# Optimization experiments

Hardware: AMD Instinct MI355X
Metric: run time of the kernel (lower is better)

The kernel has to match this reference:

```python
import jax, jax.numpy as jnp
import numpy as np

BEV_H, BEV_W, RES, ZH = 50, 50, 0.5, 0.0
IMG_H, IMG_W, STRIDE = 448, 800, 16
FH, FW = IMG_H // STRIDE, IMG_W // STRIDE  # 28, 50
NCAM, D, NL, NHEADS, NPTS = 6, 256, 2, 8, 4
NQ = BEV_H * BEV_W
EPS = 1e-5


def make_bev_grid_points():
    x = (jnp.arange(BEV_H) - (BEV_H - 1) / 2) * RES
    y = (jnp.arange(BEV_W) - (BEV_W - 1) / 2) * RES
    xx, yy = jnp.meshgrid(x, y, indexing='ij')
    return jnp.stack([xx, yy, jnp.full_like(xx, ZH)], -1).reshape(-1, 3)


def layer_norm(x, g, b):
    m = x.mean(-1, keepdims=True)
    v = x.var(-1, keepdims=True)
    return (x - m) / jnp.sqrt(v + EPS) * g + b


def group_norm(x, g, b, groups=32):
    B, C, H, W = x.shape
    xg = x.reshape(B, groups, C // groups, H, W)
    m = xg.mean((2, 3, 4), keepdims=True)
    v = xg.var((2, 3, 4), keepdims=True)
    xg = (xg - m) / jnp.sqrt(v + EPS)
    return xg.reshape(B, C, H, W) * g[None, :, None, None] + b[None, :, None, None]


def conv2d(x, w, b, stride, pad):
    y = jax.lax.conv_general_dilated(x, w, (stride, stride), ((pad, pad), (pad, pad)),
                                     dimension_numbers=('NCHW', 'OIHW', 'NCHW'))
    return y + b[None, :, None, None]


def mha(x, wq, bq, wk, bk, wv, bv, wo, bo):
    B, N, d = x.shape
    hd = d // NHEADS
    split = lambda t: t.reshape(B, N, NHEADS, hd).transpose(0, 2, 1, 3)
    q, k, v = split(x @ wq + bq), split(x @ wk + bk), split(x @ wv + bv)
    a = jax.nn.softmax(jnp.einsum('bhqd,bhkd->bhqk', q, k) * (1.0 / float(np.sqrt(hd))), axis=-1)
    o = jnp.einsum('bhqk,bhkd->bhqd', a, v).transpose(0, 2, 1, 3).reshape(B, N, d)
    return o @ wo + bo


def grid_sample(val, grid):
    # val: [C, Hf, Wf]; grid: [P, 2] in [-1, 1]; bilinear, align_corners=True, zeros padding.
    C, Hf, Wf = val.shape
    gx = (grid[:, 0] + 1.0) * 0.5 * (Wf - 1)
    gy = (grid[:, 1] + 1.0) * 0.5 * (Hf - 1)
    x0 = jnp.floor(gx)
    y0 = jnp.floor(gy)
    wx, wy = gx - x0, gy - y0
    x0i, y0i = x0.astype(jnp.int32), y0.astype(jnp.int32)
    out = jnp.zeros((C, grid.shape[0]), val.dtype)
    for dx, dy, w in ((0, 0, (1 - wx) * (1 - wy)), (1, 0, wx * (1 - wy)),
                      (0, 1, (1 - wx) * wy), (1, 1, wx * wy)):
        xi, yi = x0i + dx, y0i + dy
        ok = ((xi >= 0) & (xi < Wf) & (yi >= 0) & (yi < Hf)).astype(val.dtype)
        feat = val[:, jnp.clip(yi, 0, Hf - 1), jnp.clip(xi, 0, Wf - 1)]  # [C, P]
        out = out + (w * ok)[None, :] * feat
    return out.T  # [P, C]


def project(pts, K, E):
    # pts: [Np,3] ego-frame; K: [B,NCAM,3,3]; E: [B,NCAM,4,4]
    ph = jnp.concatenate([pts, jnp.ones((pts.shape[0], 1), pts.dtype)], -1)
    pc = jnp.einsum('bcij,pj->bcpi', E, ph)              # [B,NCAM,Np,4]
    pix = jnp.einsum('bcij,bcpj->bcpi', K, pc[..., :3])
    z = jnp.clip(pix[..., 2:3], 1e-5, None)
    uv = pix[..., :2] / z
    u, v = uv[..., 0], uv[..., 1]
    valid = (pc[..., 2] > 0) & (u >= 0) & (u < IMG_W) & (v >= 0) & (v < IMG_H)
    uvn = jnp.stack([2.0 * u / (IMG_W - 1) - 1.0, 2.0 * v / (IMG_H - 1) - 1.0], -1)
    return uvn, valid


def spatial_cross_attn(q, feats, ref, valid, ow, ob, ww, wb, vw, vb, pw, pb):
    B, Nq, d = q.shape
    vals = jnp.einsum('bnchw,cd->bndhw', feats, vw) + vb[None, None, :, None, None]
    offsets = (q @ ow + ob).reshape(B, Nq, NCAM, NHEADS, NPTS, 2)
    logits = q @ ww + wb                                  # [B,Nq,NCAM*NHEADS*NPTS]
    mask = jnp.broadcast_to(valid.transpose(0, 2, 1)[..., None],
                            (B, Nq, NCAM, NHEADS * NPTS)).reshape(B, Nq, -1)
    w = jax.nn.softmax(jnp.where(mask, logits, jnp.asarray(-1e30, logits.dtype)), axis=-1)
    w = jnp.where(mask, w, 0.0)  # == masked_fill(-inf) + softmax + nan_to_num(0)
    w = w.reshape(B, Nq, NCAM, NHEADS, NPTS)
    scale = jnp.array([2.0 / (FW - 1), 2.0 / (FH - 1)], q.dtype)
    gs = jax.vmap(grid_sample)
    out = jnp.zeros((B, Nq, d), q.dtype)
    for c in range(NCAM):  # fixed small camera loop, as in original
        pts = ref[:, c][:, :, None, None, :] + offsets[:, :, c] * scale  # [B,Nq,H,K,2]
        sampled = gs(vals[:, c], pts.reshape(B, Nq * NHEADS * NPTS, 2))
        sampled = sampled.reshape(B, Nq, NHEADS, NPTS, d)
        out = out + jnp.einsum('bqhk,bqhkd->bqd', w[:, :, c], sampled)
    return out @ pw + pb


def reference(images, intrinsics, ego_to_cam, bev_queries, bev_pos,
              bb_w0, bb_b0, bb_g0, bb_beta0, bb_w1, bb_b1, bb_g1, bb_beta1,
              bb_w2, bb_b2, bb_g2, bb_beta2, bb_w3, bb_b3, bb_g3, bb_beta3,
              bb_w4, bb_b4, bb_g4, bb_beta4,
              sa_wq, sa_bq, sa_wk, sa_bk, sa_wv, sa_bv, sa_wo, sa_bo,
              ln1_g, ln1_b, ln2_g, ln2_b, ln3_g, ln3_b,
              off_w, off_b, wt_w, wt_b, val_w, val_b, out_w, out_b,
              ffn_w1, ffn_b1, ffn_w2, ffn_b2):
    B = images.shape[0]
    x = images.reshape(B * NCAM, 3, IMG_H, IMG_W)
    for w, b, g, bt in ((bb_w0, bb_b0, bb_g0, bb_beta0), (bb_w1, bb_b1, bb_g1, bb_beta1),
                        (bb_w2, bb_b2, bb_g2, bb_beta2), (bb_w3, bb_b3, bb_g3, bb_beta3)):
        x = jax.nn.relu(group_norm(conv2d(x, w, b, 2, 1), g, bt))
    x = group_norm(conv2d(x, bb_w4, bb_b4, 1, 0), bb_g4, bb_beta4)
    feats = x.reshape(B, NCAM, D, FH, FW)
    ref_pts, valid = project(make_bev_grid_points().astype(images.dtype), intrinsics, ego_to_cam)
    q = jnp.broadcast_to((bev_queries + bev_pos)[None], (B, NQ, D))
    for l in range(NL):
        xq = layer_norm(q, ln1_g[l], ln1_b[l])
        q = q + mha(xq, sa_wq[l], sa_bq[l], sa_wk[l], sa_bk[l], sa_wv[l], sa_bv[l], sa_wo[l], sa_bo[l])
        xq = layer_norm(q, ln2_g[l], ln2_b[l])
        q = q + spatial_cross_attn(xq, feats, ref_pts, valid, off_w[l], off_b[l],
                                   wt_w[l], wt_b[l], val_w[l], val_b[l], out_w[l], out_b[l])
        xq = layer_norm(q, ln3_g[l], ln3_b[l])
        q = q + (jax.nn.gelu(xq @ ffn_w1[l] + ffn_b1[l], approximate=False) @ ffn_w2[l] + ffn_b2[l])
    return q.reshape(B, BEV_H, BEV_W, D)


def _camera_geometry():
    fx = fy = 500.0
    cx, cy = IMG_W / 2.0, IMG_H / 2.0
    K = np.array([[fx, 0, cx], [0, fy, cy], [0, 0, 1]], np.float32)
    Ks, Es = [], []
    for th in np.linspace(0, 2 * np.pi, NCAM, endpoint=False):
        f = np.array([np.cos(th), np.sin(th), 0.0])
        r = np.array([np.sin(th), -np.cos(th), 0.0])
        dn = np.array([0.0, 0.0, -1.0])
        R = np.stack([r, dn, f]).astype(np.float32)
        c = np.array([1.5 * np.cos(th), 1.5 * np.sin(th), 1.5], np.float32)
        E = np.eye(4, dtype=np.float32)
        E[:3, :3] = R
        E[:3, 3] = -R @ c
        Ks.append(K)
        Es.append(E)
    return np.stack(Ks)[None], np.stack(Es)[None]


def setup_inputs() -> dict:
    key = jax.random.key(0)
    ks = iter(jax.random.split(key, 80))
    rn = lambda shape, s: jax.random.normal(next(ks), shape, jnp.float32) * s
    K_np, E_np = _camera_geometry()
    d = {}
    d['images'] = rn((1, NCAM, 3, IMG_H, IMG_W), 1.0)
    d['intrinsics'] = jnp.asarray(K_np)
    d['ego_to_cam'] = jnp.asarray(E_np)
    d['bev_queries'] = rn((NQ, D), 0.02)
    d['bev_pos'] = rn((NQ, D), 0.02)
    for i, (co, ci) in enumerate(((64, 3), (128, 64), (256, 128), (256, 256))):
        d[f'bb_w{i}'] = rn((co, ci, 3, 3), (2.0 / (ci * 9)) ** 0.5)
        d[f'bb_b{i}'] = jnp.zeros((co,))
        d[f'bb_g{i}'] = jnp.ones((co,))
        d[f'bb_beta{i}'] = jnp.zeros((co,))
    d['bb_w4'] = rn((D, D, 1, 1), (2.0 / D) ** 0.5)
    d['bb_b4'] = jnp.zeros((D,)); d['bb_g4'] = jnp.ones((D,)); d['bb_beta4'] = jnp.zeros((D,))
    s = (1.0 / D) ** 0.5
    for n in ('q', 'k', 'v', 'o'):
        d[f'sa_w{n}'] = rn((NL, D, D), s)
        d[f'sa_b{n}'] = jnp.zeros((NL, D))
    for i in (1, 2, 3):
        d[f'ln{i}_g'] = jnp.ones((NL, D))
        d[f'ln{i}_b'] = jnp.zeros((NL, D))
    npw = NCAM * NHEADS * NPTS
    d['off_w'] = rn((NL, D, npw * 2), 0.005)  # original inits zeros; small values exercise sampling
    d['off_b'] = rn((NL, npw * 2), 0.1)
    d['wt_w'] = rn((NL, D, npw), s)
    d['wt_b'] = jnp.zeros((NL, npw))
    d['val_w'] = rn((NL, D, D), s)
    d['val_b'] = jnp.zeros((NL, D))
    d['out_w'] = rn((NL, D, D), s)
    d['out_b'] = jnp.zeros((NL, D))
    d['ffn_w1'] = rn((NL, D, 4 * D), s)
    d['ffn_b1'] = jnp.zeros((NL, 4 * D))
    d['ffn_w2'] = rn((NL, 4 * D, D), (1.0 / (4 * D)) ** 0.5)
    d['ffn_b2'] = jnp.zeros((NL, D))
    return d
```

## Files before the change

kernel.cpp:

```cpp
#include <hip/hip_runtime.h>
#include <hip/hip_bf16.h>
#include <math.h>

#define EPS 1e-5f
#define FL_SPLITS 5
#define FL_KEYS 500

typedef __attribute__((ext_vector_type(8))) short short8;
typedef __attribute__((ext_vector_type(4))) float f4;

__device__ __forceinline__ short f2s(float f) {
    union { float f; unsigned u; } v; v.f = f;
    unsigned r = (v.u + 0x7fffu + ((v.u >> 16) & 1u)) >> 16;
    return (short)r;
}
__device__ __forceinline__ unsigned packbf(float a, float b) {
    return (unsigned)(unsigned short)f2s(a) | ((unsigned)(unsigned short)f2s(b) << 16);
}
__device__ __forceinline__ float bflo(unsigned v) { union { unsigned u; float f; } t; t.u = v << 16; return t.f; }
__device__ __forceinline__ float bfhi(unsigned v) { union { unsigned u; float f; } t; t.u = v & 0xffff0000u; return t.f; }

__global__ __launch_bounds__(256) void wcast_k(const float* __restrict__ in, short* __restrict__ out, int n)
{
    int i = blockIdx.x * 256 + threadIdx.x;
    if (i < n) out[i] = f2s(in[i]);
}

__global__ __launch_bounds__(256) void wcast0_k(const float* __restrict__ in, short* __restrict__ out)
{
    int i = blockIdx.x * 256 + threadIdx.x;
    if (i >= 2048) return;
    int k = i & 31;
    out[i] = (k < 27) ? f2s(in[(i >> 5) * 27 + k]) : (short)0;
}

__global__ __launch_bounds__(256) void wreord_k(const float* __restrict__ in, short* __restrict__ out,
                                                int Cin, int n)
{
    int i = blockIdx.x * 256 + threadIdx.x;
    if (i >= n) return;
    int cin9 = Cin * 9;
    int co = i / cin9, rem = i - co * cin9;
    int ci = rem / 9, t = rem - ci * 9;
    out[(long)co * cin9 + t * Cin + ci] = f2s(in[i]);
}

__global__ __launch_bounds__(256) void wtrans_k(const float* __restrict__ in, short* __restrict__ out,
                                                int K, int N, long zstride)
{
    in  += (long)blockIdx.z * K * N;
    out += (long)blockIdx.z * zstride;
    __shared__ float t[64][65];
    int k0 = blockIdx.y * 64, n0 = blockIdx.x * 64;
    int tid = threadIdx.x;
    int cl = tid & 63, rq = tid >> 6;
    #pragma unroll
    for (int i = 0; i < 16; i++) {
        int rl = rq + i * 4;
        int k = k0 + rl, n = n0 + cl;
        t[rl][cl] = (k < K && n < N) ? in[(long)k * N + n] : 0.f;
    }
    __syncthreads();
    #pragma unroll
    for (int i = 0; i < 16; i++) {
        int nl = rq + i * 4;
        int n = n0 + nl, k = k0 + cl;
        if (n < N && k < K) out[(long)n * K + k] = f2s(t[cl][nl]);
    }
}

__global__ __launch_bounds__(256) void wtrans6_k(const float* __restrict__ s0, const float* __restrict__ s1,
                                                 const float* __restrict__ s2, const float* __restrict__ s3,
                                                 const float* __restrict__ s4, const float* __restrict__ s5,
                                                 short* __restrict__ d0, short* __restrict__ d1,
                                                 short* __restrict__ d2, short* __restrict__ d3,
                                                 short* __restrict__ d4, short* __restrict__ d5)
{
    int mat = blockIdx.z >> 1, l = blockIdx.z & 1;
    const float* in; short* out; long zs;
    if      (mat == 0) { in = s0; out = d0; zs = 196608; }
    else if (mat == 1) { in = s1; out = d1; zs = 196608; }
    else if (mat == 2) { in = s2; out = d2; zs = 196608; }
    else if (mat == 3) { in = s3; out = d3; zs = 65536; }
    else if (mat == 4) { in = s4; out = d4; zs = 65536; }
    else               { in = s5; out = d5; zs = 65536; }
    in  += (long)l * 65536;
    out += (long)l * zs;
    __shared__ float t[64][65];
    int k0 = blockIdx.y * 64, n0 = blockIdx.x * 64;
    int tid = threadIdx.x;
    int cl = tid & 63, rq = tid >> 6;
    #pragma unroll
    for (int i = 0; i < 16; i++) {
        int rl = rq + i * 4;
        t[rl][cl] = in[(long)(k0 + rl) * 256 + n0 + cl];
    }
    __syncthreads();
    #pragma unroll
    for (int i = 0; i < 16; i++) {
        int nl = rq + i * 4;
        out[(long)(n0 + nl) * 256 + k0 + cl] = f2s(t[cl][nl]);
    }
}

__global__ __launch_bounds__(256) void packb_k(const float* __restrict__ a, const float* __restrict__ b,
                                               const float* __restrict__ c, float* __restrict__ y,
                                               int na, int nb, int nc)
{
    int l = blockIdx.y;
    int j = blockIdx.x * 256 + threadIdx.x;
    int ntot = na + nb + nc;
    if (j >= ntot) return;
    float v;
    if (j < na) v = a[l * na + j];
    else if (j < na + nb) v = b[l * nb + (j - na)];
    else v = c[l * nc + (j - na - nb)];
    y[(long)l * ntot + j] = v;
}

__global__ __launch_bounds__(256) void mgemm_k(const float* __restrict__ A, int lda,
                                               const short* __restrict__ Bt,
                                               const float* __restrict__ bias,
                                               const float* __restrict__ resid,
                                               float* __restrict__ C,
                                               int M, int N, int K, int act)
{
    __shared__ __align__(16) short As[2560];
    __shared__ __align__(16) short Bs[2560];
    int tid = threadIdx.x;
    int wave = tid >> 6, lane = tid & 63;
    int wm = wave >> 1, wn = wave & 1;
    int quad = lane >> 4, l15 = lane & 15;
    int m0 = blockIdx.y * 64, n0 = blockIdx.x * 64;
    int srow = tid >> 2, skc = (tid & 3) << 3;
    f4 acc[2][2];
    #pragma unroll
    for (int i = 0; i < 2; i++) { acc[i][0] = (f4){0.f,0.f,0.f,0.f}; acc[i][1] = (f4){0.f,0.f,0.f,0.f}; }
    short8 aR, bR;
    auto loadAB = [&](int kt) {
        int gm = m0 + srow;
        short8 pk = {0, 0, 0, 0, 0, 0, 0, 0};
        if (gm < M) {
            const float4* ap = (const float4*)(A + (long)gm * lda + kt + skc);
            float4 v0 = ap[0], v1 = ap[1];
            pk[0] = f2s(v0.x); pk[1] = f2s(v0.y); pk[2] = f2s(v0.z); pk[3] = f2s(v0.w);
            pk[4] = f2s(v1.x); pk[5] = f2s(v1.y); pk[6] = f2s(v1.z); pk[7] = f2s(v1.w);
        }
        aR = pk;
        int gn = n0 + srow;
        short8 pb = {0, 0, 0, 0, 0, 0, 0, 0};
        if (gn < N) pb = *(const short8*)&Bt[(long)gn * K + kt + skc];
        bR = pb;
    };
    loadAB(0);
    for (int kt = 0; kt < K; kt += 32) {
        *(short8*)&As[srow * 40 + skc] = aR;
        *(short8*)&Bs[srow * 40 + skc] = bR;
        __syncthreads();
        if (kt + 32 < K) loadAB(kt + 32);
        short8 af[2], bf[2];
        #pragma unroll
        for (int mi = 0; mi < 2; mi++) af[mi] = *(const short8*)&As[(wm * 32 + mi * 16 + l15) * 40 + (quad << 3)];
        #pragma unroll
        for (int ni = 0; ni < 2; ni++) bf[ni] = *(const short8*)&Bs[(wn * 32 + ni * 16 + l15) * 40 + (quad << 3)];
        #pragma unroll
        for (int mi = 0; mi < 2; mi++)
            #pragma unroll
            for (int ni = 0; ni < 2; ni++)
                acc[mi][ni] = __builtin_amdgcn_mfma_f32_16x16x32_bf16(af[mi], bf[ni], acc[mi][ni], 0, 0, 0);
        __syncthreads();
    }
    #pragma unroll
    for (int mi = 0; mi < 2; mi++) {
        int row = m0 + wm * 32 + mi * 16 + quad * 4;
        #pragma unroll
        for (int ni = 0; ni < 2; ni++) {
            int col = n0 + wn * 32 + ni * 16 + l15;
            if (col >= N) continue;
            float bv = bias[col];
            #pragma unroll
            for (int r = 0; r < 4; r++) {
                int rr = row + r;
                if (rr >= M) continue;
                float v = acc[mi][ni][r] + bv;
                if (act == 2) v = 0.5f * v * (1.f + erff(v * 0.70710678118654752f));
                if (resid) v += resid[(long)rr * N + col];
                C[(long)rr * N + col] = v;
            }
        }
    }
}

__global__ __launch_bounds__(256) void mconv_k(const unsigned* __restrict__ in,
                                               const short* __restrict__ wgt,
                                               const float* __restrict__ bias,
                                               float* __restrict__ out,
                                               float2* __restrict__ parts,
                                               int c5m, int Cout, int Hin, int Win,
                                               int mode, int cpg,
                                               long istride, long ostride)
{
    in  += (long)blockIdx.z * istride;
    const int Hout = Hin >> 1, Wout = Win >> 1;
    const int HWo = Hout * Wout;
    const int HW = Hin * Win;
    const int Ktot = 288 << c5m;
    const int m5 = (1 << c5m) - 1;
    const int nsteps = 9 << c5m;
    __shared__ __align__(16) short As[2560];
    __shared__ __align__(16) short Bs[2560];
    __shared__ float2 sred[16][2];
    int tid = threadIdx.x;
    int wave = tid >> 6, lane = tid & 63;
    int wm = wave >> 1, wn = wave & 1;
    int quad = lane >> 4, l15 = lane & 15;
    int m0 = blockIdx.y * 64, n0 = blockIdx.x * 64;
    int nn = tid & 63;
    int kp0 = tid >> 6;
    int p = n0 + nn;
    int pok = p < HWo;
    int pc = pok ? p : (HWo - 1);
    int ho = pc / Wout, wo = pc - ho * Wout;
    int hb = ho * 2 - 1, wb = wo * 2 - 1;

    f4 acc[2][2];
    #pragma unroll
    for (int i = 0; i < 2; i++) { acc[i][0] = (f4){0.f,0.f,0.f,0.f}; acc[i][1] = (f4){0.f,0.f,0.f,0.f}; }

    short8 aR;
    unsigned bR[4];
    auto loadA = [&](int s) {
        int r = tid >> 2, kc = (tid & 3) << 3;
        aR = *(const short8*)&wgt[(long)(m0 + r) * Ktot + (s << 5) + kc];
    };
    auto loadB = [&](int s) {
        int t = s >> c5m;
        int kh = (t * 11) >> 5;
        int kw = t - kh * 3;
        int y = hb + kh, x = wb + kw;
        bool okp = pok && ((unsigned)y < (unsigned)Hin) && ((unsigned)x < (unsigned)Win);
        int base = (((s & m5) << 4) + kp0) * HW + y * Win + x;
        #pragma unroll
        for (int i = 0; i < 4; i++) {
            unsigned v = 0;
            if (okp) v = in[base + (i << 2) * HW];
            bR[i] = v;
        }
    };

    loadA(0); loadB(0);
    for (int s = 0; s < nsteps; s++) {
        {
            int r = tid >> 2, kc = (tid & 3) << 3;
            *(short8*)&As[r * 40 + kc] = aR;
        }
        #pragma unroll
        for (int i = 0; i < 4; i++)
            *(unsigned*)&Bs[nn * 40 + ((kp0 + (i << 2)) << 1)] = bR[i];
        __syncthreads();
        if (s + 1 < nsteps) { loadA(s + 1); loadB(s + 1); }
        short8 af[2], bf[2];
        #pragma unroll
        for (int mi = 0; mi < 2; mi++) af[mi] = *(const short8*)&As[(wm * 32 + mi * 16 + l15) * 40 + (quad << 3)];
        #pragma unroll
        for (int ni = 0; ni < 2; ni++) bf[ni] = *(const short8*)&Bs[(wn * 32 + ni * 16 + l15) * 40 + (quad << 3)];
        #pragma unroll
        for (int mi = 0; mi < 2; mi++)
            #pragma unroll
            for (int ni = 0; ni < 2; ni++)
                acc[mi][ni] = __builtin_amdgcn_mfma_f32_16x16x32_bf16(af[mi], bf[ni], acc[mi][ni], 0, 0, 0);
        __syncthreads();
    }

    if (mode == 1) {
        float* outf = out + (long)blockIdx.z * ostride;
        #pragma unroll
        for (int mi = 0; mi < 2; mi++) {
            int mbase = m0 + wm * 32 + mi * 16 + quad * 4;
            #pragma unroll
            for (int ni = 0; ni < 2; ni++) {
                int n = n0 + wn * 32 + ni * 16 + l15;
                if (n >= HWo) continue;
                #pragma unroll
                for (int r = 0; r < 4; r++) {
                    int m = mbase + r;
                    outf[(long)n * Cout + m] = acc[mi][ni][r] + bias[m];
                }
            }
        }
    } else {
        unsigned* outp = (unsigned*)out + (long)blockIdx.z * ostride;
        float ssum[2] = {0.f, 0.f}, qsum[2] = {0.f, 0.f};
        #pragma unroll
        for (int mi = 0; mi < 2; mi++) {
            int mbase = m0 + wm * 32 + mi * 16 + quad * 4;
            float b0 = bias[mbase], b1 = bias[mbase + 1], b2 = bias[mbase + 2], b3 = bias[mbase + 3];
            #pragma unroll
            for (int ni = 0; ni < 2; ni++) {
                int n = n0 + wn * 32 + ni * 16 + l15;
                if (n >= HWo) continue;
                float v0 = acc[mi][ni][0] + b0;
                float v1 = acc[mi][ni][1] + b1;
                float v2 = acc[mi][ni][2] + b2;
                float v3 = acc[mi][ni][3] + b3;
                long cp = (long)(mbase >> 1) * HWo + n;
                outp[cp]       = packbf(v0, v1);
                outp[cp + HWo] = packbf(v2, v3);
                ssum[mi] += v0 + v1 + v2 + v3;
                qsum[mi] += v0 * v0 + v1 * v1 + v2 * v2 + v3 * v3;
            }
        }
        #pragma unroll
        for (int mi = 0; mi < 2; mi++) {
            #pragma unroll
            for (int off = 1; off < 16; off <<= 1) {
                ssum[mi] += __shfl_xor(ssum[mi], off, 16);
                qsum[mi] += __shfl_xor(qsum[mi], off, 16);
            }
        }
        if (l15 == 0) {
            #pragma unroll
            for (int mi = 0; mi < 2; mi++)
                sred[wm * 8 + mi * 4 + quad][wn] = make_float2(ssum[mi], qsum[mi]);
        }
        __syncthreads();
        int ng = 64 / cpg;
        int qpg = cpg >> 2;
        if (tid < ng) {
            float s = 0.f, q = 0.f;
            for (int u = 0; u < qpg; u++) {
                float2 a = sred[(tid * cpg >> 2) + u][0];
                float2 b = sred[(tid * cpg >> 2) + u][1];
                s += a.x + b.x; q += a.y + b.y;
            }
            int gabs = m0 / cpg + tid;
            parts[((long)blockIdx.z * 32 + gabs) * 1400 + blockIdx.x] = make_float2(s, q);
        }
    }
}

__global__ __launch_bounds__(256) void conv0f_k(const float* __restrict__ img,
                                                const short* __restrict__ wgt,
                                                const float* __restrict__ bias,
                                                unsigned* __restrict__ outp,
                                                float2* __restrict__ parts,
                                                long istride, long ostride)
{
    img  += (long)blockIdx.z * istride;
    outp += (long)blockIdx.z * ostride;
    const int HWo = 89600;
    __shared__ __align__(16) short As[2560];
    __shared__ __align__(16) short Bs[2560];
    __shared__ float2 sred[32][2];
    int tid = threadIdx.x;
    int wave = tid >> 6, lane = tid & 63;
    int wm = wave >> 1, wn = wave & 1;
    int quad = lane >> 4, l15 = lane & 15;
    int n0 = blockIdx.x * 64;
    int srow = tid >> 2, skc = (tid & 3) << 3;
    *(short8*)&As[srow * 40 + skc] = *(const short8*)&wgt[srow * 32 + skc];
    {
        int p = n0 + srow;
        int ho = p / 400, wo = p - ho * 400;
        int hb = ho * 2 - 1, wb = wo * 2 - 1;
        short8 pb;
        #pragma unroll
        for (int j = 0; j < 8; j++) {
            int k = skc + j;
            float v = 0.f;
            if (k < 27) {
                int ci = (k < 9) ? 0 : (k < 18 ? 1 : 2);
                int t = k - ci * 9;
                int kh = (t < 3) ? 0 : (t < 6 ? 1 : 2);
                int kw = t - kh * 3;
                int y = hb + kh, x = wb + kw;
                if ((unsigned)y < 448u && (unsigned)x < 800u)
                    v = img[ci * 358400 + y * 800 + x];
            }
            pb[j] = f2s(v);
        }
        *(short8*)&Bs[srow * 40 + skc] = pb;
    }
    __syncthreads();
    f4 acc[2][2];
    #pragma unroll
    for (int i = 0; i < 2; i++) { acc[i][0] = (f4){0.f,0.f,0.f,0.f}; acc[i][1] = (f4){0.f,0.f,0.f,0.f}; }
    short8 af[2], bf[2];
    #pragma unroll
    for (int mi = 0; mi < 2; mi++) af[mi] = *(const short8*)&As[(wm * 32 + mi * 16 + l15) * 40 + (quad << 3)];
    #pragma unroll
    for (int ni = 0; ni < 2; ni++) bf[ni] = *(const short8*)&Bs[(wn * 32 + ni * 16 + l15) * 40 + (quad << 3)];
    #pragma unroll
    for (int mi = 0; mi < 2; mi++)
        #pragma unroll
        for (int ni = 0; ni < 2; ni++)
            acc[mi][ni] = __builtin_amdgcn_mfma_f32_16x16x32_bf16(af[mi], bf[ni], acc[mi][ni], 0, 0, 0);
    #pragma unroll
    for (int mi = 0; mi < 2; mi++) {
        int mbase = wm * 32 + mi * 16 + quad * 4;
        float b0 = bias[mbase], b1 = bias[mbase + 1], b2 = bias[mbase + 2], b3 = bias[mbase + 3];
        float s0 = 0.f, q0 = 0.f, s1 = 0.f, q1 = 0.f;
        #pragma unroll
        for (int ni = 0; ni < 2; ni++) {
            int n = n0 + wn * 32 + ni * 16 + l15;
            float v0 = acc[mi][ni][0] + b0;
            float v1 = acc[mi][ni][1] + b1;
            float v2 = acc[mi][ni][2] + b2;
            float v3 = acc[mi][ni][3] + b3;
            long cp = (long)(mbase >> 1) * HWo + n;
            outp[cp]       = packbf(v0, v1);
            outp[cp + HWo] = packbf(v2, v3);
            s0 += v0 + v1; q0 += v0 * v0 + v1 * v1;
            s1 += v2 + v3; q1 += v2 * v2 + v3 * v3;
        }
        #pragma unroll
        for (int off = 1; off < 16; off <<= 1) {
            s0 += __shfl_xor(s0, off, 16); q0 += __shfl_xor(q0, off, 16);
            s1 += __shfl_xor(s1, off, 16); q1 += __shfl_xor(q1, off, 16);
        }
        if (l15 == 0) {
            int pi = wm * 16 + mi * 8 + quad * 2;
            sred[pi][wn]     = make_float2(s0, q0);
            sred[pi + 1][wn] = make_float2(s1, q1);
        }
    }
    __syncthreads();
    if (tid < 32) {
        float2 a = sred[tid][0], b = sred[tid][1];
        parts[((long)blockIdx.z * 32 + tid) * 1400 + blockIdx.x] = make_float2(a.x + b.x, a.y + b.y);
    }
}

__global__ __launch_bounds__(256) void gnfin_k(const float2* __restrict__ parts,
                                               float* __restrict__ gnstats, int nx, float invN)
{
    int g = blockIdx.x, cam = blockIdx.y;
    const float2* pb = parts + ((long)cam * 32 + g) * 1400;
    float s = 0.f, q = 0.f;
    for (int i = threadIdx.x; i < nx; i += 256) {
        float2 v = pb[i];
        s += v.x; q += v.y;
    }
    __shared__ float rs[256], rq[256];
    rs[threadIdx.x] = s; rq[threadIdx.x] = q;
    __syncthreads();
    for (int o = 128; o > 0; o >>= 1) {
        if (threadIdx.x < o) { rs[threadIdx.x] += rs[threadIdx.x + o]; rq[threadIdx.x] += rq[threadIdx.x + o]; }
        __syncthreads();
    }
    if (threadIdx.x == 0) {
        float mean = rs[0] * invN;
        float var  = rq[0] * invN - mean * mean;
        gnstats[(cam * 32 + g) * 2]     = mean;
        gnstats[(cam * 32 + g) * 2 + 1] = rsqrtf(var + EPS);
    }
}

__global__ __launch_bounds__(256) void pairapply_k(unsigned* __restrict__ x,
                                                   const float* __restrict__ gamma,
                                                   const float* __restrict__ beta,
                                                   const float* __restrict__ gnstats,
                                                   int HW, int cpg, long zstride)
{
    x       += (long)blockIdx.z * zstride;
    gnstats += (long)blockIdx.z * 64;
    int idx4 = (blockIdx.x * 256 + threadIdx.x) * 4;
    int cp = idx4 / HW;
    int c0 = cp * 2;
    int g = c0 / cpg;
    float mean = gnstats[g * 2], rstd = gnstats[g * 2 + 1];
    float sa = rstd * gamma[c0],     ba = beta[c0]     - mean * sa;
    float sb = rstd * gamma[c0 + 1], bb = beta[c0 + 1] - mean * sb;
    uint4 v = *(uint4*)&x[idx4];
    unsigned* vp = (unsigned*)&v;
    #pragma unroll
    for (int j = 0; j < 4; j++) {
        float lo = fmaxf(bflo(vp[j]) * sa + ba, 0.f);
        float hi = fmaxf(bfhi(vp[j]) * sb + bb, 0.f);
        vp[j] = packbf(lo, hi);
    }
    *(uint4*)&x[idx4] = v;
}

__global__ __launch_bounds__(256) void gn_stats_hwd_k(const float* __restrict__ x, float* __restrict__ stats)
{
    x += (long)blockIdx.y * 358400;
    stats += blockIdx.y * 64;
    int g = blockIdx.x;
    float s = 0.f, s2 = 0.f;
    for (int i = threadIdx.x; i < 1400 * 8; i += blockDim.x) {
        int p = i >> 3, c = g * 8 + (i & 7);
        float v = x[(long)p * 256 + c];
        s += v; s2 += v * v;
    }
    __shared__ float rs[256], rq[256];
    rs[threadIdx.x] = s; rq[threadIdx.x] = s2;
    __syncthreads();
    for (int o = 128; o > 0; o >>= 1) {
        if (threadIdx.x < o) { rs[threadIdx.x] += rs[threadIdx.x + o]; rq[threadIdx.x] += rq[threadIdx.x + o]; }
        __syncthreads();
    }
    if (threadIdx.x == 0) {
        float mean = rs[0] / 11200.f;
        float var  = rq[0] / 11200.f - mean * mean;
        stats[g * 2]     = mean;
        stats[g * 2 + 1] = rsqrtf(var + EPS);
    }
}

__global__ __launch_bounds__(256) void gn_apply_hwd_k(float* __restrict__ x,
                                                      const float* __restrict__ gamma,
                                                      const float* __restrict__ beta,
                                                      const float* __restrict__ stats,
                                                      int relu)
{
    x += (long)blockIdx.y * 358400;
    stats += blockIdx.y * 64;
    long i4 = ((long)blockIdx.x * 256 + threadIdx.x) * 4;
    int c = (int)(i4 & 255);
    int g = c >> 3;
    float4 v  = *(float4*)&x[i4];
    float4 gm = *(const float4*)&gamma[c];
    float4 bt = *(const float4*)&beta[c];
    float m = stats[g * 2], rs = stats[g * 2 + 1];
    v.x = (v.x - m) * rs * gm.x + bt.x;
    v.y = (v.y - m) * rs * gm.y + bt.y;
    v.z = (v.z - m) * rs * gm.z + bt.z;
    v.w = (v.w - m) * rs * gm.w + bt.w;
    if (relu) {
        v.x = fmaxf(v.x, 0.f); v.y = fmaxf(v.y, 0.f);
        v.z = fmaxf(v.z, 0.f); v.w = fmaxf(v.w, 0.f);
    }
    *(float4*)&x[i4] = v;
}

__global__ __launch_bounds__(256) void project_k(const float* __restrict__ Kin,
                                                 const float* __restrict__ Ein,
                                                 float* __restrict__ refp, int* __restrict__ valid)
{
    int idx = blockIdx.x * blockDim.x + threadIdx.x;
    if (idx >= 2500 * 6) return;
    int c = idx % 6, q = idx / 6;
    int i = q / 50, j = q % 50;
    float px = (i - 24.5f) * 0.5f;
    float py = (j - 24.5f) * 0.5f;
    const float* E = Ein + c * 16;
    float pc[4];
    #pragma unroll
    for (int r = 0; r < 4; r++)
        pc[r] = E[r * 4 + 0] * px + E[r * 4 + 1] * py + E[r * 4 + 3];
    const float* Km = Kin + c * 9;
    float pix[3];
    #pragma unroll
    for (int r = 0; r < 3; r++)
        pix[r] = Km[r * 3 + 0] * pc[0] + Km[r * 3 + 1] * pc[1] + Km[r * 3 + 2] * pc[2];
    float z = fmaxf(pix[2], 1e-5f);
    float u = pix[0] / z, v = pix[1] / z;
    int ok = (pc[2] > 0.f) && (u >= 0.f) && (u < 800.f) && (v >= 0.f) && (v < 448.f);
    refp[(long)idx * 2 + 0] = 2.f * u / 799.f - 1.f;
    refp[(long)idx * 2 + 1] = 2.f * v / 447.f - 1.f;
    valid[idx] = ok;
}

__global__ __launch_bounds__(256) void qinit_k(const float* __restrict__ a, const float* __restrict__ b,
                                               float* __restrict__ y)
{
    int i = blockIdx.x * blockDim.x + threadIdx.x;
    if (i >= 2500 * 256) return;
    y[i] = a[i] + b[i];
}

__global__ __launch_bounds__(256) void ln_k(const float* __restrict__ x,
                                            const float* __restrict__ g, const float* __restrict__ b,
                                            float* __restrict__ y)
{
    int row  = blockIdx.x * 4 + (threadIdx.x >> 6);
    int lane = threadIdx.x & 63;
    if (row >= 2500) return;
    const float* xp = x + (long)row * 256;
    float v[4];
    #pragma unroll
    for (int i = 0; i < 4; i++) v[i] = xp[lane + 64 * i];
    float s  = v[0] + v[1] + v[2] + v[3];
    float s2 = v[0] * v[0] + v[1] * v[1] + v[2] * v[2] + v[3] * v[3];
    #pragma unroll
    for (int o = 32; o > 0; o >>= 1) { s += __shfl_xor(s, o, 64); s2 += __shfl_xor(s2, o, 64); }
    float mean = s * (1.f / 256.f);
    float var  = s2 * (1.f / 256.f) - mean * mean;
    float rstd = rsqrtf(var + EPS);
    #pragma unroll
    for (int i = 0; i < 4; i++) {
        int cc = lane + 64 * i;
        y[(long)row * 256 + cc] = (v[i] - mean) * rstd * g[cc] + b[cc];
    }
}

__global__ __launch_bounds__(256) void flash2_k(const float* __restrict__ Q,
                                                const float* __restrict__ K,
                                                const float* __restrict__ V,
                                                int ld,
                                                float* __restrict__ Opart,
                                                float* __restrict__ MLpart)
{
    const int h  = blockIdx.y;
    const int q0 = blockIdx.x * 64;
    const int sp = blockIdx.z;
    const int kstart = sp * FL_KEYS, kend = kstart + FL_KEYS;
    const int tid = threadIdx.x;
    const int wave = tid >> 6, lane = tid & 63;
    const int quad = lane >> 4, l15 = lane & 15;
    __shared__ __align__(16) short Qs[64 * 40];
    __shared__ __align__(16) short Ks[64 * 40];
    __shared__ __align__(16) short Vt[32 * 72];
    __shared__ __align__(16) short Ps[64 * 72];
    const float scale = 0.17677669529663687f;
    {
        int row = tid >> 2, kc = (tid & 3) << 3;
        int qi = q0 + row;
        short8 pk = {0, 0, 0, 0, 0, 0, 0, 0};
        if (qi < 2500) {
            const float4* qp = (const float4*)(Q + (long)qi * ld + h * 32 + kc);
            float4 v0 = qp[0], v1 = qp[1];
            pk[0] = f2s(v0.x * scale); pk[1] = f2s(v0.y * scale); pk[2] = f2s(v0.z * scale); pk[3] = f2s(v0.w * scale);
            pk[4] = f2s(v1.x * scale); pk[5] = f2s(v1.y * scale); pk[6] = f2s(v1.z * scale); pk[7] = f2s(v1.w * scale);
        }
        *(short8*)&Qs[row * 40 + kc] = pk;
    }
    __syncthreads();
    short8 aq = *(const short8*)&Qs[(wave * 16 + l15) * 40 + (quad << 3)];
    float m[4], l[4];
    f4 oacc[2];
    #pragma unroll
    for (int r = 0; r < 4; r++) { m[r] = -INFINITY; l[r] = 0.f; }
    oacc[0] = (f4){0.f, 0.f, 0.f, 0.f};
    oacc[1] = (f4){0.f, 0.f, 0.f, 0.f};
    for (int kb = kstart; kb < kend; kb += 64) {
        __syncthreads();
        {
            int row = tid >> 2, kc = (tid & 3) << 3;
            int ki = kb + row;
            short8 pk = {0, 0, 0, 0, 0, 0, 0, 0};
            float vv[8] = {0.f, 0.f, 0.f, 0.f, 0.f, 0.f, 0.f, 0.f};
            if (ki < kend) {
                const float4* kp = (const float4*)(K + (long)ki * ld + h * 32 + kc);
                float4 a0 = kp[0], a1 = kp[1];
                pk[0] = f2s(a0.x); pk[1] = f2s(a0.y); pk[2] = f2s(a0.z); pk[3] = f2s(a0.w);
                pk[4] = f2s(a1.x); pk[5] = f2s(a1.y); pk[6] = f2s(a1.z); pk[7] = f2s(a1.w);
                const float4* vp = (const float4*)(V + (long)ki * ld + h * 32 + kc);
                float4 b0 = vp[0], b1 = vp[1];
                vv[0] = b0.x; vv[1] = b0.y; vv[2] = b0.z; vv[3] = b0.w;
                vv[4] = b1.x; vv[5] = b1.y; vv[6] = b1.z; vv[7] = b1.w;
            }
            *(short8*)&Ks[row * 40 + kc] = pk;
            #pragma unroll
            for (int j = 0; j < 8; j++) Vt[(kc + j) * 72 + row] = f2s(vv[j]);
        }
        __syncthreads();
        f4 sa[4];
        #pragma unroll
        for (int ni = 0; ni < 4; ni++) {
            short8 bk = *(const short8*)&Ks[(ni * 16 + l15) * 40 + (quad << 3)];
            sa[ni] = __builtin_amdgcn_mfma_f32_16x16x32_bf16(aq, bk, (f4){0.f, 0.f, 0.f, 0.f}, 0, 0, 0);
        }
        float sv[4][4];
        #pragma unroll
        for (int ni = 0; ni < 4; ni++) {
            bool colok = (kb + ni * 16 + l15) < kend;
            #pragma unroll
            for (int r = 0; r < 4; r++) sv[ni][r] = colok ? sa[ni][r] : -1e30f;
        }
        float p[4][4];
        #pragma unroll
        for (int r = 0; r < 4; r++) {
            float rm = fmaxf(fmaxf(sv[0][r], sv[1][r]), fmaxf(sv[2][r], sv[3][r]));
            #pragma unroll
            for (int off = 1; off < 16; off <<= 1) rm = fmaxf(rm, __shfl_xor(rm, off, 16));
            float mn = fmaxf(m[r], rm);
            float alpha = __expf(m[r] - mn);
            float rs = 0.f;
            #pragma unroll
            for (int ni = 0; ni < 4; ni++) { p[ni][r] = __expf(sv[ni][r] - mn); rs += p[ni][r]; }
            #pragma unroll
            for (int off = 1; off < 16; off <<= 1) rs += __shfl_xor(rs, off, 16);
            l[r] = l[r] * alpha + rs;
            oacc[0][r] *= alpha; oacc[1][r] *= alpha;
            m[r] = mn;
        }
        #pragma unroll
        for (int ni = 0; ni < 4; ni++)
            #pragma unroll
            for (int r = 0; r < 4; r++)
                Ps[(wave * 16 + quad * 4 + r) * 72 + ni * 16 + l15] = f2s(p[ni][r]);
        #pragma unroll
        for (int kh = 0; kh < 2; kh++) {
            short8 ap = *(const short8*)&Ps[(wave * 16 + l15) * 72 + kh * 32 + (quad << 3)];
            #pragma unroll
            for (int ni = 0; ni < 2; ni++) {
                short8 bv = *(const short8*)&Vt[(ni * 16 + l15) * 72 + kh * 32 + (quad << 3)];
                oacc[ni] = __builtin_amdgcn_mfma_f32_16x16x32_bf16(ap, bv, oacc[ni], 0, 0, 0);
            }
        }
    }
    #pragma unroll
    for (int r = 0; r < 4; r++) {
        int qi = q0 + wave * 16 + quad * 4 + r;
        if (qi < 2500) {
            long ob = ((long)sp * 2500 + qi) * 256 + h * 32;
            Opart[ob + l15]      = oacc[0][r];
            Opart[ob + 16 + l15] = oacc[1][r];
            if (l15 == 0) {
                long mb = (((long)sp * 2500 + qi) * 8 + h) * 2;
                MLpart[mb]     = m[r];
                MLpart[mb + 1] = l[r];
            }
        }
    }
}

__global__ __launch_bounds__(256) void flashmerge_k(const float* __restrict__ Opart,
                                                    const float* __restrict__ MLpart,
                                                    float* __restrict__ O)
{
    int q = blockIdx.x, d = threadIdx.x;
    int h = d >> 5;
    float ms[FL_SPLITS], ls[FL_SPLITS];
    float mg = -INFINITY;
    #pragma unroll
    for (int s = 0; s < FL_SPLITS; s++) {
        long mb = (((long)s * 2500 + q) * 8 + h) * 2;
        ms[s] = MLpart[mb];
        ls[s] = MLpart[mb + 1];
        mg = fmaxf(mg, ms[s]);
    }
    float lsum = 0.f, osum = 0.f;
    #pragma unroll
    for (int s = 0; s < FL_SPLITS; s++) {
        float w = __expf(ms[s] - mg);
        lsum += ls[s] * w;
        osum += Opart[((long)s * 2500 + q) * 256 + d] * w;
    }
    O[(long)q * 256 + d] = osum / lsum;
}

__global__ __launch_bounds__(64) void scasoftmax_k(float* __restrict__ logits, int ld,
                                                   const int* __restrict__ valid)
{
    int q = blockIdx.x, lane = threadIdx.x;
    float v[3]; int mk[3];
    #pragma unroll
    for (int i = 0; i < 3; i++) {
        int idx = i * 64 + lane;
        int c = idx >> 5;
        mk[i] = valid[q * 6 + c];
        v[i] = mk[i] ? logits[(long)q * ld + idx] : -1e30f;
    }
    float mx = fmaxf(fmaxf(v[0], v[1]), v[2]);
    #pragma unroll
    for (int o = 32; o > 0; o >>= 1) mx = fmaxf(mx, __shfl_xor(mx, o, 64));
    float e[3]; float s = 0.f;
    #pragma unroll
    for (int i = 0; i < 3; i++) { e[i] = expf(v[i] - mx); s += e[i]; }
    #pragma unroll
    for (int o = 32; o > 0; o >>= 1) s += __shfl_xor(s, o, 64);
    float inv = 1.f / s;
    #pragma unroll
    for (int i = 0; i < 3; i++)
        logits[(long)q * ld + i * 64 + lane] = mk[i] ? e[i] * inv : 0.f;
}

__global__ __launch_bounds__(256) void sample_k(const float* __restrict__ vals,
                                                const float* __restrict__ offs, int ld,
                                                const float* __restrict__ wts,
                                                const float* __restrict__ refp,
                                                const int* __restrict__ valid,
                                                float* __restrict__ out)
{
    int q = blockIdx.x, d = threadIdx.x;
    __shared__ float s_cw[6][32][4];
    __shared__ int   s_idx[6][32][4];
    if (d < 192) {
        int c = d >> 5, pt = d & 31;
        if (valid[q * 6 + c]) {
            float ox = offs[(long)q * ld + (c * 32 + pt) * 2 + 0];
            float oy = offs[(long)q * ld + (c * 32 + pt) * 2 + 1];
            float px = refp[(q * 6 + c) * 2 + 0] + ox * (2.f / 49.f);
            float py = refp[(q * 6 + c) * 2 + 1] + oy * (2.f / 27.f);
            float gx = (px + 1.f) * 0.5f * 49.f;
            float gy = (py + 1.f) * 0.5f * 27.f;
            float x0f = floorf(gx), y0f = floorf(gy);
            float wx = gx - x0f, wy = gy - y0f;
            int x0 = (int)x0f, y0 = (int)y0f;
            float wgt = wts[(long)q * ld + c * 32 + pt];
            float cw[4] = {(1.f - wx) * (1.f - wy), wx * (1.f - wy), (1.f - wx) * wy, wx * wy};
            const int dxs[4] = {0, 1, 0, 1};
            const int dys[4] = {0, 0, 1, 1};
            #pragma unroll
            for (int k2 = 0; k2 < 4; k2++) {
                int xi = x0 + dxs[k2], yi = y0 + dys[k2];
                bool ok = (xi >= 0) && (xi < 50) && (yi >= 0) && (yi < 28);
                s_cw[c][pt][k2]  = ok ? cw[k2] * wgt : 0.f;
                s_idx[c][pt][k2] = ok ? (yi * 50 + xi) * 256 : 0;
            }
        }
    }
    __syncthreads();
    float acc = 0.f;
    for (int c = 0; c < 6; c++) {
        if (!valid[q * 6 + c]) continue;
        const float* vb = vals + (long)c * 358400 + d;
        for (int pt = 0; pt < 32; pt++) {
            #pragma unroll
            for (int k2 = 0; k2 < 4; k2++) {
                float cwv = s_cw[c][pt][k2];
                if (cwv != 0.f) acc += cwv * vb[s_idx[c][pt][k2]];
            }
        }
    }
    out[(long)q * 256 + d] = acc;
}

extern "C" void kernel_launch(void* const* d_in, const int* in_sizes, int n_in,
                              void* d_out, int out_size, void* d_ws, size_t ws_size,
                              hipStream_t stream)
{
    const float* images = (const float*)d_in[0];
    const float* intr   = (const float*)d_in[1];
    const float* e2c    = (const float*)d_in[2];
    const float* bevq   = (const float*)d_in[3];
    const float* bevp   = (const float*)d_in[4];
    const float* bbw[5]    = {(const float*)d_in[5],  (const float*)d_in[9],  (const float*)d_in[13], (const float*)d_in[17], (const float*)d_in[21]};
    const float* bbb[5]    = {(const float*)d_in[6],  (const float*)d_in[10], (const float*)d_in[14], (const float*)d_in[18], (const float*)d_in[22]};
    const float* bbg[5]    = {(const float*)d_in[7],  (const float*)d_in[11], (const float*)d_in[15], (const float*)d_in[19], (const float*)d_in[23]};
    const float* bbbeta[5] = {(const float*)d_in[8],  (const float*)d_in[12], (const float*)d_in[16], (const float*)d_in[20], (const float*)d_in[24]};
    const float* sa_wq = (const float*)d_in[25]; const float* sa_bq = (const float*)d_in[26];
    const float* sa_wk = (const float*)d_in[27]; const float* sa_bk = (const float*)d_in[28];
    const float* sa_wv = (const float*)d_in[29]; const float* sa_bv = (const float*)d_in[30];
    const float* sa_wo = (const float*)d_in[31]; const float* sa_bo = (const float*)d_in[32];
    const float* ln1g = (const float*)d_in[33]; const float* ln1b = (const float*)d_in[34];
    const float* ln2g = (const float*)d_in[35]; const float* ln2b = (const float*)d_in[36];
    const float* ln3g = (const float*)d_in[37]; const float* ln3b = (const float*)d_in[38];
    const float* offw = (const float*)d_in[39]; const float* offb = (const float*)d_in[40];
    const float* wtw  = (const float*)d_in[41]; const float* wtb  = (const float*)d_in[42];
    const float* valw = (const float*)d_in[43]; const float* valb = (const float*)d_in[44];
    const float* outw = (const float*)d_in[45]; const float* outb = (const float*)d_in[46];
    const float* fw1  = (const float*)d_in[47]; const float* fb1  = (const float*)d_in[48];
    const float* fw2  = (const float*)d_in[49]; const float* fb2  = (const float*)d_in[50];

    auto needB = [](long ncb) -> unsigned long long {
        return (unsigned long long)(ncb * 8601600L + 6681600L) * 4ULL + 6307840ULL + (1 << 20);
    };
    int ncb = 1;
    if      ((unsigned long long)ws_size >= needB(6)) ncb = 6;
    else if ((unsigned long long)ws_size >= needB(3)) ncb = 3;
    else if ((unsigned long long)ws_size >= needB(2)) ncb = 2;

    float* ws = (float*)d_ws;
    float* A     = ws; ws += (long)ncb * 5734400;
    float* Bu    = ws; ws += (long)ncb * 2867200;
    float* f3bH  = ws; ws += 2560000;
    float* feats = ws; ws += 2150400;
    float* qbuf  = ws; ws += 640000;
    float* xq    = ws; ws += 640000;
    float* bO    = ws; ws += 640000;
    float* refp  = ws; ws += 30016;
    int*   validb = (int*)ws; ws += 15040;
    float* stats = ws; ws += 384;
    float* gnst  = ws; ws += 3072;
    float* qkvb  = ws; ws += 1536;
    float* owb   = ws; ws += 1152;
    short* sb = (short*)ws;
    short* cw0b = sb; sb += 2048;
    short* cw1b = sb; sb += 73728;
    short* cw2b = sb; sb += 294912;
    short* cw3b = sb; sb += 589824;
    short* cw4b = sb; sb += 65536;
    short* qkvT = sb; sb += 393216;
    short* owT  = sb; sb += 131072;
    short* valT = sb; sb += 131072;
    short* outT = sb; sb += 131072;
    short* offwtT = sb; sb += 294912;
    short* f1T  = sb; sb += 524288;
    short* f2T  = sb; sb += 524288;
    float*  feats3 = f3bH;
    float*  bH     = f3bH;
    float*  bQKV   = A;
    float*  OP     = A + 1920000;
    float*  bOW    = A + 1920000;
    float*  valsb  = Bu;
    float*  MLp    = Bu + 2150400;
    unsigned* Bbf0 = (unsigned*)A;
    unsigned* Bbf1 = (unsigned*)Bu;
    float2* partsP = (float2*)feats;

    auto mgemm = [&](const float* Ain, int lda, const short* Bt, const float* bias, const float* resid,
                     float* C, int M, int N, int K, int act) {
        dim3 g((N + 63) / 64, (M + 63) / 64);
        mgemm_k<<<g, 256, 0, stream>>>(Ain, lda, Bt, bias, resid, C, M, N, K, act);
    };

    wcast0_k<<<8, 256, 0, stream>>>(bbw[0], cw0b);
    wreord_k<<<(73728 + 255) / 256, 256, 0, stream>>>(bbw[1], cw1b, 64, 73728);
    wreord_k<<<(294912 + 255) / 256, 256, 0, stream>>>(bbw[2], cw2b, 128, 294912);
    wreord_k<<<(589824 + 255) / 256, 256, 0, stream>>>(bbw[3], cw3b, 256, 589824);
    wcast_k<<<(65536 + 255) / 256, 256, 0, stream>>>(bbw[4], cw4b, 65536);
    wtrans6_k<<<dim3(4, 4, 12), 256, 0, stream>>>(sa_wq, sa_wk, sa_wv, sa_wo, valw, outw,
                                                  qkvT, qkvT + 65536, qkvT + 131072, owT, valT, outT);
    wtrans_k<<<dim3(6, 4, 2), 256, 0, stream>>>(offw, offwtT,         256, 384,  147456);
    wtrans_k<<<dim3(3, 4, 2), 256, 0, stream>>>(wtw,  offwtT + 98304, 256, 192,  147456);
    wtrans_k<<<dim3(16, 4, 2), 256, 0, stream>>>(fw1, f1T, 256, 1024, 262144);
    wtrans_k<<<dim3(4, 16, 2), 256, 0, stream>>>(fw2, f2T, 1024, 256, 262144);
    packb_k<<<dim3(3, 2), 256, 0, stream>>>(sa_bq, sa_bk, sa_bv, qkvb, 256, 256, 256);
    packb_k<<<dim3(3, 2), 256, 0, stream>>>(offb, wtb, nullptr, owb, 384, 192, 0);

    project_k<<<(15000 + 255) / 256, 256, 0, stream>>>(intr, e2c, refp, validb);

    for (int c0 = 0; c0 < 6; c0 += ncb) {
        const float* img = images + (long)c0 * 1075200;
        conv0f_k<<<dim3(1400, 1, ncb), 256, 0, stream>>>(img, cw0b, bbb[0], Bbf0, partsP,
                                                         1075200L, 2867200L);
        gnfin_k<<<dim3(32, ncb), 256, 0, stream>>>(partsP, gnst, 1400, 1.f / 179200.f);
        pairapply_k<<<dim3(2800, 1, ncb), 256, 0, stream>>>(Bbf0, bbg[0], bbbeta[0], gnst, 89600, 2, 2867200L);
        mconv_k<<<dim3(350, 2, ncb), 256, 0, stream>>>(Bbf0, cw1b, bbb[1], (float*)Bbf1, partsP,
                                                       1, 128, 224, 400, 2, 4, 2867200L, 1433600L);
        gnfin_k<<<dim3(32, ncb), 256, 0, stream>>>(partsP, gnst, 350, 1.f / 89600.f);
        pairapply_k<<<dim3(1400, 1, ncb), 256, 0, stream>>>(Bbf1, bbg[1], bbbeta[1], gnst, 22400, 4, 1433600L);
        mconv_k<<<dim3(88, 4, ncb), 256, 0, stream>>>(Bbf1, cw2b, bbb[2], (float*)Bbf0, partsP,
                                                      2, 256, 112, 200, 2, 8, 1433600L, 716800L);
        gnfin_k<<<dim3(32, ncb), 256, 0, stream>>>(partsP, gnst, 88, 1.f / 44800.f);
        pairapply_k<<<dim3(700, 1, ncb), 256, 0, stream>>>(Bbf0, bbg[2], bbbeta[2], gnst, 5600, 8, 716800L);
        mconv_k<<<dim3(22, 4, ncb), 256, 0, stream>>>(Bbf0, cw3b, bbb[3], feats3 + (long)c0 * 358400, nullptr,
                                                      3, 256, 56, 100, 1, 0, 716800L, 358400L);
    }
    gn_stats_hwd_k<<<dim3(32, 6), 256, 0, stream>>>(feats3, stats);
    gn_apply_hwd_k<<<dim3(350, 6), 256, 0, stream>>>(feats3, bbg[3], bbbeta[3], stats, 1);
    mgemm(feats3, 256, cw4b, bbb[4], nullptr, feats, 8400, 256, 256, 0);
    gn_stats_hwd_k<<<dim3(32, 6), 256, 0, stream>>>(feats, stats);
    gn_apply_hwd_k<<<dim3(350, 6), 256, 0, stream>>>(feats, bbg[4], bbbeta[4], stats, 0);

    qinit_k<<<2500, 256, 0, stream>>>(bevq, bevp, qbuf);

    for (int l = 0; l < 2; l++) {
        long o1 = (long)l * 256;

        ln_k<<<625, 256, 0, stream>>>(qbuf, ln1g + o1, ln1b + o1, xq);
        mgemm(xq, 256, qkvT + l * 196608, qkvb + l * 768, nullptr, bQKV, 2500, 768, 256, 0);
        flash2_k<<<dim3(40, 8, FL_SPLITS), 256, 0, stream>>>(bQKV, bQKV + 256, bQKV + 512, 768, OP, MLp);
        flashmerge_k<<<2500, 256, 0, stream>>>(OP, MLp, bO);
        mgemm(bO, 256, owT + l * 65536, sa_bo + o1, qbuf, qbuf, 2500, 256, 256, 0);

        ln_k<<<625, 256, 0, stream>>>(qbuf, ln2g + o1, ln2b + o1, xq);
        mgemm(feats, 256, valT + l * 65536, valb + o1, nullptr, valsb, 8400, 256, 256, 0);
        mgemm(xq, 256, offwtT + l * 147456, owb + l * 576, nullptr, bOW, 2500, 576, 256, 0);
        scasoftmax_k<<<2500, 64, 0, stream>>>(bOW + 384, 576, validb);
        sample_k<<<2500, 256, 0, stream>>>(valsb, bOW, 576, bOW + 384, refp, validb, bO);
        mgemm(bO, 256, outT + l * 65536, outb + o1, qbuf, qbuf, 2500, 256, 256, 0);

        ln_k<<<625, 256, 0, stream>>>(qbuf, ln3g + o1, ln3b + o1, xq);
        mgemm(xq, 256, f1T + l * 262144, fb1 + (long)l * 1024, nullptr, bH, 2500, 1024, 256, 2);
        mgemm(bH, 1024, f2T + l * 262144, fb2 + o1, qbuf,
              (l == 1) ? (float*)d_out : qbuf, 2500, 256, 1024, 0);
    }
}
```

Before: 1.031 ms.

## Remap conv workgroups XCD-aware and vectorize B-tile LDS stores

The strided conv kernel now flattens its grid into one dimension and remaps workgroup ids so that consecutive logical tiles, including the output-channel tiles that read the same spatial input patch, are dispatched to the same XCD. The goal is more L2 reuse of the input activations. Each thread also now loads four consecutive channel pairs, so it can write its B-tile slice to LDS with one 16-byte store instead of four 4-byte stores. The remap adds integer index arithmetic per block, and the new global load pattern changes coalescing across threads.

```diff
diff --git a/kernel.cpp b/kernel.cpp
--- a/kernel.cpp
+++ b/kernel.cpp
@@ -197,10 +197,20 @@
                                                float* __restrict__ out,
                                                float2* __restrict__ parts,
                                                int c5m, int Cout, int Hin, int Win,
-                                               int mode, int cpg,
+                                               int mode, int cpg, int ctshift,
                                                long istride, long ostride)
 {
-    in  += (long)blockIdx.z * istride;
+    int lin = blockIdx.x + gridDim.x * blockIdx.z;
+    int nwgT = gridDim.x * gridDim.z;
+    int xcd = lin & 7, seq = lin >> 3;
+    int qd = nwgT >> 3, rd = nwgT & 7;
+    int wgid = (xcd < rd ? xcd * (qd + 1) : rd * (qd + 1) + (xcd - rd) * qd) + seq;
+    int cam = wgid / gridDim.x;
+    int rem = wgid - cam * gridDim.x;
+    int couttile = rem & ((1 << ctshift) - 1);
+    int spatial = rem >> ctshift;
+
+    in  += (long)cam * istride;
     const int Hout = Hin >> 1, Wout = Win >> 1;
     const int HWo = Hout * Wout;
     const int HW = Hin * Win;
@@ -214,7 +224,7 @@
     int wave = tid >> 6, lane = tid & 63;
     int wm = wave >> 1, wn = wave & 1;
     int quad = lane >> 4, l15 = lane & 15;
-    int m0 = blockIdx.y * 64, n0 = blockIdx.x * 64;
+    int m0 = couttile << 6, n0 = spatial << 6;
     int nn = tid & 63;
     int kp0 = tid >> 6;
     int p = n0 + nn;
@@ -239,11 +249,11 @@
         int kw = t - kh * 3;
         int y = hb + kh, x = wb + kw;
         bool okp = pok && ((unsigned)y < (unsigned)Hin) && ((unsigned)x < (unsigned)Win);
-        int base = (((s & m5) << 4) + kp0) * HW + y * Win + x;
+        int base = (((s & m5) << 4) + (kp0 << 2)) * HW + y * Win + x;
         #pragma unroll
         for (int i = 0; i < 4; i++) {
             unsigned v = 0;
-            if (okp) v = in[base + (i << 2) * HW];
+            if (okp) v = in[base + i * HW];
             bR[i] = v;
         }
     };
@@ -254,9 +264,7 @@
             int r = tid >> 2, kc = (tid & 3) << 3;
             *(short8*)&As[r * 40 + kc] = aR;
         }
-        #pragma unroll
-        for (int i = 0; i < 4; i++)
-            *(unsigned*)&Bs[nn * 40 + ((kp0 + (i << 2)) << 1)] = bR[i];
+        *(uint4*)&Bs[nn * 40 + (kp0 << 3)] = *(uint4*)bR;
         __syncthreads();
         if (s + 1 < nsteps) { loadA(s + 1); loadB(s + 1); }
         short8 af[2], bf[2];
@@ -273,7 +281,7 @@
     }
 
     if (mode == 1) {
-        float* outf = out + (long)blockIdx.z * ostride;
+        float* outf = out + (long)cam * ostride;
         #pragma unroll
         for (int mi = 0; mi < 2; mi++) {
             int mbase = m0 + wm * 32 + mi * 16 + quad * 4;
@@ -289,7 +297,7 @@
             }
         }
     } else {
-        unsigned* outp = (unsigned*)out + (long)blockIdx.z * ostride;
+        unsigned* outp = (unsigned*)out + (long)cam * ostride;
         float ssum[2] = {0.f, 0.f}, qsum[2] = {0.f, 0.f};
         #pragma unroll
         for (int mi = 0; mi < 2; mi++) {
@@ -334,7 +342,7 @@
                 s += a.x + b.x; q += a.y + b.y;
             }
             int gabs = m0 / cpg + tid;
-            parts[((long)blockIdx.z * 32 + gabs) * 1400 + blockIdx.x] = make_float2(s, q);
+            parts[((long)cam * 32 + gabs) * 1400 + spatial] = make_float2(s, q);
         }
     }
 }
@@ -920,16 +928,16 @@
                                                          1075200L, 2867200L);
         gnfin_k<<<dim3(32, ncb), 256, 0, stream>>>(partsP, gnst, 1400, 1.f / 179200.f);
         pairapply_k<<<dim3(2800, 1, ncb), 256, 0, stream>>>(Bbf0, bbg[0], bbbeta[0], gnst, 89600, 2, 2867200L);
-        mconv_k<<<dim3(350, 2, ncb), 256, 0, stream>>>(Bbf0, cw1b, bbb[1], (float*)Bbf1, partsP,
-                                                       1, 128, 224, 400, 2, 4, 2867200L, 1433600L);
+        mconv_k<<<dim3(700, 1, ncb), 256, 0, stream>>>(Bbf0, cw1b, bbb[1], (float*)Bbf1, partsP,
+                                                       1, 128, 224, 400, 2, 4, 1, 2867200L, 1433600L);
         gnfin_k<<<dim3(32, ncb), 256, 0, stream>>>(partsP, gnst, 350, 1.f / 89600.f);
         pairapply_k<<<dim3(1400, 1, ncb), 256, 0, stream>>>(Bbf1, bbg[1], bbbeta[1], gnst, 22400, 4, 1433600L);
-        mconv_k<<<dim3(88, 4, ncb), 256, 0, stream>>>(Bbf1, cw2b, bbb[2], (float*)Bbf0, partsP,
-                                                      2, 256, 112, 200, 2, 8, 1433600L, 716800L);
+        mconv_k<<<dim3(352, 1, ncb), 256, 0, stream>>>(Bbf1, cw2b, bbb[2], (float*)Bbf0, partsP,
+                                                       2, 256, 112, 200, 2, 8, 2, 1433600L, 716800L);
         gnfin_k<<<dim3(32, ncb), 256, 0, stream>>>(partsP, gnst, 88, 1.f / 44800.f);
         pairapply_k<<<dim3(700, 1, ncb), 256, 0, stream>>>(Bbf0, bbg[2], bbbeta[2], gnst, 5600, 8, 716800L);
-        mconv_k<<<dim3(22, 4, ncb), 256, 0, stream>>>(Bbf0, cw3b, bbb[3], feats3 + (long)c0 * 358400, nullptr,
-                                                      3, 256, 56, 100, 1, 0, 716800L, 358400L);
+        mconv_k<<<dim3(88, 1, ncb), 256, 0, stream>>>(Bbf0, cw3b, bbb[3], feats3 + (long)c0 * 358400, nullptr,
+                                                      3, 256, 56, 100, 1, 0, 2, 716800L, 358400L);
     }
     gn_stats_hwd_k<<<dim3(32, 6), 256, 0, stream>>>(feats3, stats);
     gn_apply_hwd_k<<<dim3(350, 6), 256, 0, stream>>>(feats3, bbg[3], bbbeta[3], stats, 1);
```

Result: faster. 990.7 us (-3.9%).
